# Optimization experiments

Measured on AMD Instinct MI355X. Metric: run time of the kernel, lower is better.

The kernel has to match this reference:

```python
import jax, jax.numpy as jnp
import numpy as np

B, TE, TD, D, U = 8, 256, 256, 256, 256


def setup_inputs() -> dict:
    key = jax.random.key(0)
    k1, k2, k3, k4, k5 = jax.random.split(key, 5)
    glorot = lambda k, shape: jax.random.uniform(
        k, shape, jnp.float32,
        -np.sqrt(6.0 / (shape[0] + shape[1])), np.sqrt(6.0 / (shape[0] + shape[1])))
    return {
        "en_seq": jax.random.normal(k1, (B, TE, D), jnp.float32),
        "de_seq": jax.random.normal(k2, (B, TD, D), jnp.float32),
        "w_en": glorot(k3, (D, U)),
        "w_de": glorot(k4, (D, U)),
        "nu": glorot(k5, (U, 1)),
    }


def reference(en_seq, de_seq, w_en, w_de, nu):
    # Additive co-attention scores.
    ae = jnp.einsum('bte,eu->btu', en_seq, w_en)          # (B, Te, U)
    ad = jnp.einsum('bsd,du->bsu', de_seq, w_de)          # (B, Td, U)
    # co_m[b, td, te, u] = ae[b, te, u] + ad[b, td, u]  (matches K.repeat / repeat_elements layout)
    co = jnp.tanh(ad[:, :, None, :] + ae[:, None, :, :])  # (B, Td, Te, U)
    mu = jnp.einsum('bstu,ul->bst', co, nu)               # (B, Td, Te)
    alphas = jax.nn.softmax(mu, axis=-1)                  # softmax over en time
    max_mu = jnp.max(mu, axis=-1)                         # (B, Td)
    max_alphas = jax.nn.softmax(max_mu, axis=-1)          # softmax over de time
    h_hat = jnp.sum(de_seq * max_alphas[..., None], axis=1)  # (B, Dd)
    sum_en = jnp.einsum('bst,bte->bse', alphas, en_seq)      # (B, Td, De)
    output = jnp.concatenate(
        [de_seq, sum_en, de_seq * sum_en, de_seq * h_hat[:, None, :]], axis=-1)
    return output  # (B, Td, 4*D)
```

## Files before the change

### kernel.cpp

```cpp
#include <hip/hip_runtime.h>

#define B_   8
#define TE_  256
#define TD_  256
#define D_   256
#define U_   256

#define AE_OFF    0
#define AD_OFF    524288
#define SUMEN_OFF 1048576
#define MAXMU_OFF 1572864

__device__ __forceinline__ float fexp2(float x) {
#if __has_builtin(__builtin_amdgcn_exp2f)
  return __builtin_amdgcn_exp2f(x);
#else
  return exp2f(x);
#endif
}
__device__ __forceinline__ float frcp(float x) {
#if __has_builtin(__builtin_amdgcn_rcpf)
  return __builtin_amdgcn_rcpf(x);
#else
  return 1.0f / x;
#endif
}

#define LOG2E_F 1.4426950408889634f
#define TWO_LOG2E_F 2.8853900817779268f

__global__ __launch_bounds__(256) void coatt_ka_proj(
    const float* __restrict__ en, const float* __restrict__ de,
    const float* __restrict__ w_en, const float* __restrict__ w_de,
    float* __restrict__ ws) {
  const int which = blockIdx.z;
  const float* __restrict__ A = which ? de : en;
  const float* __restrict__ W = which ? w_de : w_en;
  float* __restrict__ out = ws + (which ? AD_OFF : AE_OFF);
  const int rowBase = blockIdx.y * 64;
  const int colBase = blockIdx.x * 64;
  __shared__ float As[16][68];
  __shared__ float Bs[16][68];
  const int tid = threadIdx.x;
  const int tx = tid & 15, ty = tid >> 4;
  float acc[4][4] = {};
  for (int k0 = 0; k0 < D_; k0 += 16) {
    {
      const int r = tid >> 2;
      const int c = (tid & 3) * 4;
      const float4 a4 = *(const float4*)&A[(rowBase + r) * D_ + k0 + c];
      As[c + 0][r] = a4.x; As[c + 1][r] = a4.y;
      As[c + 2][r] = a4.z; As[c + 3][r] = a4.w;
      const int kk = tid >> 4;
      const int cc = (tid & 15) * 4;
      *(float4*)&Bs[kk][cc] = *(const float4*)&W[(k0 + kk) * U_ + colBase + cc];
    }
    __syncthreads();
#pragma unroll
    for (int k = 0; k < 16; ++k) {
      float av[4], bv[4];
      *(float4*)av = *(const float4*)&As[k][ty * 4];
      *(float4*)bv = *(const float4*)&Bs[k][tx * 4];
#pragma unroll
      for (int i = 0; i < 4; ++i)
#pragma unroll
        for (int j = 0; j < 4; ++j)
          acc[i][j] = fmaf(av[i], bv[j], acc[i][j]);
    }
    __syncthreads();
  }
#pragma unroll
  for (int i = 0; i < 4; ++i) {
    float4 o;
    o.x = fexp2(acc[i][0] * TWO_LOG2E_F);
    o.y = fexp2(acc[i][1] * TWO_LOG2E_F);
    o.z = fexp2(acc[i][2] * TWO_LOG2E_F);
    o.w = fexp2(acc[i][3] * TWO_LOG2E_F);
    *(float4*)&out[(rowBase + ty * 4 + i) * U_ + colBase + tx * 4] = o;
  }
}

__global__ __launch_bounds__(256) void coatt_kb_fused(
    const float* __restrict__ nu, const float* __restrict__ en,
    float* __restrict__ ws) {
  const float* __restrict__ Ee = ws + AE_OFF;
  const float* __restrict__ Ed = ws + AD_OFF;
  float* __restrict__ sum_en = ws + SUMEN_OFF;
  float* __restrict__ maxmu = ws + MAXMU_OFF;
  const int b = blockIdx.y;
  const int sBase = blockIdx.x * 4;
  const int tid = threadIdx.x;
  const int w = tid >> 6, lane = tid & 63;

  __shared__ float EdS[4][256];
  __shared__ float NUs[256];
  __shared__ float EeT[16][260];
  __shared__ float Mu[4][260];

  {
    const int r = tid >> 6, c4 = tid & 63;
    *(float4*)&EdS[r][c4 * 4] =
        *(const float4*)&Ed[(b * TD_ + sBase + r) * U_ + c4 * 4];
    NUs[tid] = -2.0f * nu[tid];
  }
  __syncthreads();

  float acc0 = 0.f, acc1 = 0.f, acc2 = 0.f, acc3 = 0.f;
  const int t = tid;
  for (int u0 = 0; u0 < U_; u0 += 16) {
#pragma unroll
    for (int k = 0; k < 4; ++k) {
      const int f = tid + 256 * k;
      const int tt = f >> 2, c = f & 3;
      const float4 v = *(const float4*)&Ee[(b * TE_ + tt) * U_ + u0 + c * 4];
      EeT[c * 4 + 0][tt] = v.x;
      EeT[c * 4 + 1][tt] = v.y;
      EeT[c * 4 + 2][tt] = v.z;
      EeT[c * 4 + 3][tt] = v.w;
    }
    __syncthreads();
#pragma unroll
    for (int uq = 0; uq < 4; ++uq) {
      float nv[4];
      *(float4*)nv = *(const float4*)&NUs[u0 + uq * 4];
      float ee[4];
#pragma unroll
      for (int j = 0; j < 4; ++j) ee[j] = EeT[uq * 4 + j][t];
      float e0[4], e1[4], e2[4], e3[4];
      *(float4*)e0 = *(const float4*)&EdS[0][u0 + uq * 4];
      *(float4*)e1 = *(const float4*)&EdS[1][u0 + uq * 4];
      *(float4*)e2 = *(const float4*)&EdS[2][u0 + uq * 4];
      *(float4*)e3 = *(const float4*)&EdS[3][u0 + uq * 4];
#pragma unroll
      for (int j = 0; j < 4; ++j) {
        acc0 = fmaf(nv[j], frcp(fmaf(e0[j], ee[j], 1.0f)), acc0);
        acc1 = fmaf(nv[j], frcp(fmaf(e1[j], ee[j], 1.0f)), acc1);
        acc2 = fmaf(nv[j], frcp(fmaf(e2[j], ee[j], 1.0f)), acc2);
        acc3 = fmaf(nv[j], frcp(fmaf(e3[j], ee[j], 1.0f)), acc3);
      }
    }
    __syncthreads();
  }

  Mu[0][t] = acc0;
  Mu[1][t] = acc1;
  Mu[2][t] = acc2;
  Mu[3][t] = acc3;
  __syncthreads();
  {
    float4 v = *(const float4*)&Mu[w][lane * 4];
    float m = fmaxf(fmaxf(v.x, v.y), fmaxf(v.z, v.w));
#pragma unroll
    for (int off = 32; off > 0; off >>= 1) m = fmaxf(m, __shfl_xor(m, off));
    float4 e;
    e.x = fexp2((v.x - m) * LOG2E_F);
    e.y = fexp2((v.y - m) * LOG2E_F);
    e.z = fexp2((v.z - m) * LOG2E_F);
    e.w = fexp2((v.w - m) * LOG2E_F);
    float sm = (e.x + e.y) + (e.z + e.w);
#pragma unroll
    for (int off = 32; off > 0; off >>= 1) sm += __shfl_xor(sm, off);
    const float inv = frcp(sm);
    e.x *= inv; e.y *= inv; e.z *= inv; e.w *= inv;
    *(float4*)&Mu[w][lane * 4] = e;
    if (lane == 0) maxmu[b * TD_ + sBase + w] = m;
  }
  __syncthreads();

  float4 p0 = {0, 0, 0, 0}, p1 = {0, 0, 0, 0}, p2 = {0, 0, 0, 0}, p3 = {0, 0, 0, 0};
  for (int t0 = 0; t0 < TE_; t0 += 16) {
#pragma unroll
    for (int k = 0; k < 4; ++k) {
      const int f = tid + 256 * k;
      const int r = f >> 6, c4 = f & 63;
      *(float4*)&EeT[r][c4 * 4] =
          *(const float4*)&en[(b * TE_ + t0 + r) * D_ + c4 * 4];
    }
    __syncthreads();
    float a0[4], a1[4], a2[4], a3[4];
    *(float4*)a0 = *(const float4*)&Mu[0][t0 + w * 4];
    *(float4*)a1 = *(const float4*)&Mu[1][t0 + w * 4];
    *(float4*)a2 = *(const float4*)&Mu[2][t0 + w * 4];
    *(float4*)a3 = *(const float4*)&Mu[3][t0 + w * 4];
#pragma unroll
    for (int j = 0; j < 4; ++j) {
      const float4 env = *(const float4*)&EeT[w * 4 + j][lane * 4];
      p0.x = fmaf(a0[j], env.x, p0.x); p0.y = fmaf(a0[j], env.y, p0.y);
      p0.z = fmaf(a0[j], env.z, p0.z); p0.w = fmaf(a0[j], env.w, p0.w);
      p1.x = fmaf(a1[j], env.x, p1.x); p1.y = fmaf(a1[j], env.y, p1.y);
      p1.z = fmaf(a1[j], env.z, p1.z); p1.w = fmaf(a1[j], env.w, p1.w);
      p2.x = fmaf(a2[j], env.x, p2.x); p2.y = fmaf(a2[j], env.y, p2.y);
      p2.z = fmaf(a2[j], env.z, p2.z); p2.w = fmaf(a2[j], env.w, p2.w);
      p3.x = fmaf(a3[j], env.x, p3.x); p3.y = fmaf(a3[j], env.y, p3.y);
      p3.z = fmaf(a3[j], env.z, p3.z); p3.w = fmaf(a3[j], env.w, p3.w);
    }
    __syncthreads();
  }
  {
    float* RED = &EeT[0][0];
    *(float4*)&RED[((w * 4 + 0) * 64 + lane) * 4] = p0;
    *(float4*)&RED[((w * 4 + 1) * 64 + lane) * 4] = p1;
    *(float4*)&RED[((w * 4 + 2) * 64 + lane) * 4] = p2;
    *(float4*)&RED[((w * 4 + 3) * 64 + lane) * 4] = p3;
    __syncthreads();
    const int s = tid >> 6, l = tid & 63;
    float4 sum = {0, 0, 0, 0};
#pragma unroll
    for (int ww = 0; ww < 4; ++ww) {
      const float4 q = *(const float4*)&RED[((ww * 4 + s) * 64 + l) * 4];
      sum.x += q.x; sum.y += q.y; sum.z += q.z; sum.w += q.w;
    }
    *(float4*)&sum_en[(b * TD_ + sBase + s) * D_ + l * 4] = sum;
  }
}

__global__ __launch_bounds__(256) void coatt_kc_out(
    const float* __restrict__ de, const float* __restrict__ ws,
    float* __restrict__ out) {
  const float* __restrict__ sum_en = ws + SUMEN_OFF;
  const float* __restrict__ maxmu = ws + MAXMU_OFF;
  const int b = blockIdx.y;
  const int sBase = blockIdx.x * 8;
  const int tid = threadIdx.x;
  const int w = tid >> 6, lane = tid & 63;
  __shared__ float malpha[256];
  __shared__ float red[8];
  __shared__ float hhL[256];
  const float v = maxmu[b * TD_ + tid];
  float m = v;
#pragma unroll
  for (int off = 32; off > 0; off >>= 1) m = fmaxf(m, __shfl_xor(m, off));
  if (lane == 0) red[w] = m;
  __syncthreads();
  m = fmaxf(fmaxf(red[0], red[1]), fmaxf(red[2], red[3]));
  const float e = fexp2((v - m) * LOG2E_F);
  float sm = e;
#pragma unroll
  for (int off = 32; off > 0; off >>= 1) sm += __shfl_xor(sm, off);
  if (lane == 0) red[4 + w] = sm;
  __syncthreads();
  sm = (red[4] + red[5]) + (red[6] + red[7]);
  malpha[tid] = e * frcp(sm);
  __syncthreads();
  float hh = 0.f;
#pragma unroll 8
  for (int s = 0; s < TD_; ++s)
    hh = fmaf(de[(b * TD_ + s) * D_ + tid], malpha[s], hh);
  hhL[tid] = hh;
  __syncthreads();
#pragma unroll
  for (int pass = 0; pass < 2; ++pass) {
    const int s = sBase + pass * 4 + w;
    const float4 d4 = *(const float4*)&de[(b * TD_ + s) * D_ + lane * 4];
    const float4 se4 = *(const float4*)&sum_en[(b * TD_ + s) * D_ + lane * 4];
    const float4 hh4 = *(const float4*)&hhL[lane * 4];
    float* o = out + (size_t)(b * TD_ + s) * (4 * D_);
    *(float4*)&o[lane * 4] = d4;
    *(float4*)&o[D_ + lane * 4] = se4;
    float4 pr;
    pr.x = d4.x * se4.x; pr.y = d4.y * se4.y;
    pr.z = d4.z * se4.z; pr.w = d4.w * se4.w;
    *(float4*)&o[2 * D_ + lane * 4] = pr;
    float4 q;
    q.x = d4.x * hh4.x; q.y = d4.y * hh4.y;
    q.z = d4.z * hh4.z; q.w = d4.w * hh4.w;
    *(float4*)&o[3 * D_ + lane * 4] = q;
  }
}

extern "C" void kernel_launch(void* const* d_in, const int* in_sizes, int n_in,
                              void* d_out, int out_size, void* d_ws, size_t ws_size,
                              hipStream_t stream) {
  (void)in_sizes; (void)n_in; (void)out_size; (void)ws_size;
  const float* en   = (const float*)d_in[0];
  const float* de   = (const float*)d_in[1];
  const float* w_en = (const float*)d_in[2];
  const float* w_de = (const float*)d_in[3];
  const float* nu   = (const float*)d_in[4];
  float* out = (float*)d_out;
  float* ws  = (float*)d_ws;

  coatt_ka_proj<<<dim3(4, 32, 2), 256, 0, stream>>>(en, de, w_en, w_de, ws);
  coatt_kb_fused<<<dim3(64, 8), 256, 0, stream>>>(nu, en, ws);
  coatt_kc_out<<<dim3(32, 8), 256, 0, stream>>>(de, ws, out);
}
```

Measured before the change: 132.4 us.

## Split fused attention kernel into mu/softmax, h-hat and output kernels with transposed Ee

The projection kernel now double-buffers 32-wide K tiles through registers and writes the encoder exponentials transposed (b,u,t), so the mu kernel reads them coalesced straight from global memory without LDS staging. The fused kernel is split into a mu+softmax kernel that writes alphas to workspace, an h-hat kernel parallelised over d, and an output kernel that computes sum_en from alphas and en, then writes all four output segments. This removes the LDS transposes and barriers and spreads the h-hat reduction over more blocks. In exchange it adds a kernel launch and a global round trip for alphas, and en is reread per block.

```diff
diff --git a/kernel.cpp b/kernel.cpp
--- a/kernel.cpp
+++ b/kernel.cpp
@@ -6,10 +6,11 @@
 #define D_   256
 #define U_   256
 
-#define AE_OFF    0
-#define AD_OFF    524288
-#define SUMEN_OFF 1048576
+#define EET_OFF   0
+#define ED_OFF    524288
+#define ALPHA_OFF 1048576
 #define MAXMU_OFF 1572864
+#define HH_OFF    1574912
 
 __device__ __forceinline__ float fexp2(float x) {
 #if __has_builtin(__builtin_amdgcn_exp2f)
@@ -29,203 +30,189 @@
 #define LOG2E_F 1.4426950408889634f
 #define TWO_LOG2E_F 2.8853900817779268f
 
-__global__ __launch_bounds__(256) void coatt_ka_proj(
+__global__ __launch_bounds__(256) void coatt_k1_proj(
     const float* __restrict__ en, const float* __restrict__ de,
     const float* __restrict__ w_en, const float* __restrict__ w_de,
     float* __restrict__ ws) {
   const int which = blockIdx.z;
   const float* __restrict__ A = which ? de : en;
   const float* __restrict__ W = which ? w_de : w_en;
-  float* __restrict__ out = ws + (which ? AD_OFF : AE_OFF);
   const int rowBase = blockIdx.y * 64;
   const int colBase = blockIdx.x * 64;
-  __shared__ float As[16][68];
-  __shared__ float Bs[16][68];
+  __shared__ float As[2][32][68];
+  __shared__ float Bs[2][32][68];
   const int tid = threadIdx.x;
   const int tx = tid & 15, ty = tid >> 4;
+
+  const int aRow0 = tid >> 3, aC4 = tid & 7;
+  const int bK0 = tid >> 4, bC4 = tid & 15;
+  float4 aR[2], bR[2];
+
+#pragma unroll
+  for (int kk = 0; kk < 2; ++kk) {
+    aR[kk] = *(const float4*)&A[(rowBase + aRow0 + 32 * kk) * D_ + aC4 * 4];
+    bR[kk] = *(const float4*)&W[(bK0 + 16 * kk) * U_ + colBase + bC4 * 4];
+  }
+#pragma unroll
+  for (int kk = 0; kk < 2; ++kk) {
+    float v[4]; *(float4*)v = aR[kk];
+#pragma unroll
+    for (int j = 0; j < 4; ++j) As[0][aC4 * 4 + j][aRow0 + 32 * kk] = v[j];
+    *(float4*)&Bs[0][bK0 + 16 * kk][bC4 * 4] = bR[kk];
+  }
+  __syncthreads();
+
   float acc[4][4] = {};
-  for (int k0 = 0; k0 < D_; k0 += 16) {
-    {
-      const int r = tid >> 2;
-      const int c = (tid & 3) * 4;
-      const float4 a4 = *(const float4*)&A[(rowBase + r) * D_ + k0 + c];
-      As[c + 0][r] = a4.x; As[c + 1][r] = a4.y;
-      As[c + 2][r] = a4.z; As[c + 3][r] = a4.w;
-      const int kk = tid >> 4;
-      const int cc = (tid & 15) * 4;
-      *(float4*)&Bs[kk][cc] = *(const float4*)&W[(k0 + kk) * U_ + colBase + cc];
+#define K1_COMPUTE(BUF)                                            \
+  _Pragma("unroll")                                                \
+  for (int k = 0; k < 32; ++k) {                                   \
+    float av[4], bv[4];                                            \
+    *(float4*)av = *(const float4*)&As[BUF][k][ty * 4];            \
+    *(float4*)bv = *(const float4*)&Bs[BUF][k][tx * 4];            \
+    _Pragma("unroll")                                              \
+    for (int i = 0; i < 4; ++i)                                    \
+      _Pragma("unroll")                                            \
+      for (int j = 0; j < 4; ++j)                                  \
+        acc[i][j] = fmaf(av[i], bv[j], acc[i][j]);                 \
+  }
+
+  for (int kc = 0; kc < 7; ++kc) {
+    const int k0 = (kc + 1) * 32;
+#pragma unroll
+    for (int kk = 0; kk < 2; ++kk) {
+      aR[kk] = *(const float4*)&A[(rowBase + aRow0 + 32 * kk) * D_ + k0 + aC4 * 4];
+      bR[kk] = *(const float4*)&W[(k0 + bK0 + 16 * kk) * U_ + colBase + bC4 * 4];
+    }
+    const int cur = kc & 1, nxt = cur ^ 1;
+    K1_COMPUTE(cur)
+#pragma unroll
+    for (int kk = 0; kk < 2; ++kk) {
+      float v[4]; *(float4*)v = aR[kk];
+#pragma unroll
+      for (int j = 0; j < 4; ++j) As[nxt][aC4 * 4 + j][aRow0 + 32 * kk] = v[j];
+      *(float4*)&Bs[nxt][bK0 + 16 * kk][bC4 * 4] = bR[kk];
     }
     __syncthreads();
-#pragma unroll
-    for (int k = 0; k < 16; ++k) {
-      float av[4], bv[4];
-      *(float4*)av = *(const float4*)&As[k][ty * 4];
-      *(float4*)bv = *(const float4*)&Bs[k][tx * 4];
-#pragma unroll
-      for (int i = 0; i < 4; ++i)
-#pragma unroll
-        for (int j = 0; j < 4; ++j)
-          acc[i][j] = fmaf(av[i], bv[j], acc[i][j]);
-    }
+  }
+  K1_COMPUTE(1)
+  __syncthreads();
+
+  if (which) {
+    float* __restrict__ out = ws + ED_OFF;
+#pragma unroll
+    for (int i = 0; i < 4; ++i) {
+      float4 o;
+      o.x = fexp2(acc[i][0] * TWO_LOG2E_F);
+      o.y = fexp2(acc[i][1] * TWO_LOG2E_F);
+      o.z = fexp2(acc[i][2] * TWO_LOG2E_F);
+      o.w = fexp2(acc[i][3] * TWO_LOG2E_F);
+      *(float4*)&out[(rowBase + ty * 4 + i) * U_ + colBase + tx * 4] = o;
+    }
+  } else {
+    float* Cs = &As[0][0][0];
+#pragma unroll
+    for (int i = 0; i < 4; ++i)
+#pragma unroll
+      for (int j = 0; j < 4; ++j)
+        Cs[(tx * 4 + j) * 68 + ty * 4 + i] = fexp2(acc[i][j] * TWO_LOG2E_F);
     __syncthreads();
-  }
-#pragma unroll
-  for (int i = 0; i < 4; ++i) {
-    float4 o;
-    o.x = fexp2(acc[i][0] * TWO_LOG2E_F);
-    o.y = fexp2(acc[i][1] * TWO_LOG2E_F);
-    o.z = fexp2(acc[i][2] * TWO_LOG2E_F);
-    o.w = fexp2(acc[i][3] * TWO_LOG2E_F);
-    *(float4*)&out[(rowBase + ty * 4 + i) * U_ + colBase + tx * 4] = o;
-  }
-}
-
-__global__ __launch_bounds__(256) void coatt_kb_fused(
-    const float* __restrict__ nu, const float* __restrict__ en,
-    float* __restrict__ ws) {
-  const float* __restrict__ Ee = ws + AE_OFF;
-  const float* __restrict__ Ed = ws + AD_OFF;
-  float* __restrict__ sum_en = ws + SUMEN_OFF;
+    float* __restrict__ out = ws + EET_OFF;
+    const int b = rowBase >> 8, t0 = rowBase & 255;
+#pragma unroll
+    for (int kk = 0; kk < 4; ++kk) {
+      const int q = tid + 256 * kk;
+      const int uc = q >> 4, tq = q & 15;
+      const float4 v = *(const float4*)&Cs[uc * 68 + tq * 4];
+      *(float4*)&out[(size_t)(b * U_ + colBase + uc) * TE_ + t0 + tq * 4] = v;
+    }
+  }
+}
+
+__global__ __launch_bounds__(256) void coatt_k2_mu(
+    const float* __restrict__ nu, float* __restrict__ ws) {
+  const float* __restrict__ EeT = ws + EET_OFF;
+  const float* __restrict__ Ed = ws + ED_OFF;
+  float* __restrict__ alphas = ws + ALPHA_OFF;
   float* __restrict__ maxmu = ws + MAXMU_OFF;
   const int b = blockIdx.y;
   const int sBase = blockIdx.x * 4;
   const int tid = threadIdx.x;
   const int w = tid >> 6, lane = tid & 63;
-
-  __shared__ float EdS[4][256];
-  __shared__ float NUs[256];
-  __shared__ float EeT[16][260];
-  __shared__ float Mu[4][260];
-
-  {
-    const int r = tid >> 6, c4 = tid & 63;
-    *(float4*)&EdS[r][c4 * 4] =
-        *(const float4*)&Ed[(b * TD_ + sBase + r) * U_ + c4 * 4];
-    NUs[tid] = -2.0f * nu[tid];
-  }
-  __syncthreads();
+  const float* __restrict__ Ee_b = EeT + (size_t)b * U_ * TE_ + tid;
+  const float* __restrict__ Ed_b = Ed + (size_t)(b * TD_ + sBase) * U_;
 
   float acc0 = 0.f, acc1 = 0.f, acc2 = 0.f, acc3 = 0.f;
-  const int t = tid;
-  for (int u0 = 0; u0 < U_; u0 += 16) {
-#pragma unroll
-    for (int k = 0; k < 4; ++k) {
-      const int f = tid + 256 * k;
-      const int tt = f >> 2, c = f & 3;
-      const float4 v = *(const float4*)&Ee[(b * TE_ + tt) * U_ + u0 + c * 4];
-      EeT[c * 4 + 0][tt] = v.x;
-      EeT[c * 4 + 1][tt] = v.y;
-      EeT[c * 4 + 2][tt] = v.z;
-      EeT[c * 4 + 3][tt] = v.w;
-    }
-    __syncthreads();
-#pragma unroll
-    for (int uq = 0; uq < 4; ++uq) {
-      float nv[4];
-      *(float4*)nv = *(const float4*)&NUs[u0 + uq * 4];
-      float ee[4];
-#pragma unroll
-      for (int j = 0; j < 4; ++j) ee[j] = EeT[uq * 4 + j][t];
-      float e0[4], e1[4], e2[4], e3[4];
-      *(float4*)e0 = *(const float4*)&EdS[0][u0 + uq * 4];
-      *(float4*)e1 = *(const float4*)&EdS[1][u0 + uq * 4];
-      *(float4*)e2 = *(const float4*)&EdS[2][u0 + uq * 4];
-      *(float4*)e3 = *(const float4*)&EdS[3][u0 + uq * 4];
-#pragma unroll
-      for (int j = 0; j < 4; ++j) {
-        acc0 = fmaf(nv[j], frcp(fmaf(e0[j], ee[j], 1.0f)), acc0);
-        acc1 = fmaf(nv[j], frcp(fmaf(e1[j], ee[j], 1.0f)), acc1);
-        acc2 = fmaf(nv[j], frcp(fmaf(e2[j], ee[j], 1.0f)), acc2);
-        acc3 = fmaf(nv[j], frcp(fmaf(e3[j], ee[j], 1.0f)), acc3);
-      }
-    }
-    __syncthreads();
-  }
-
-  Mu[0][t] = acc0;
-  Mu[1][t] = acc1;
-  Mu[2][t] = acc2;
-  Mu[3][t] = acc3;
-  __syncthreads();
-  {
-    float4 v = *(const float4*)&Mu[w][lane * 4];
-    float m = fmaxf(fmaxf(v.x, v.y), fmaxf(v.z, v.w));
-#pragma unroll
-    for (int off = 32; off > 0; off >>= 1) m = fmaxf(m, __shfl_xor(m, off));
-    float4 e;
-    e.x = fexp2((v.x - m) * LOG2E_F);
-    e.y = fexp2((v.y - m) * LOG2E_F);
-    e.z = fexp2((v.z - m) * LOG2E_F);
-    e.w = fexp2((v.w - m) * LOG2E_F);
-    float sm = (e.x + e.y) + (e.z + e.w);
-#pragma unroll
-    for (int off = 32; off > 0; off >>= 1) sm += __shfl_xor(sm, off);
-    const float inv = frcp(sm);
-    e.x *= inv; e.y *= inv; e.z *= inv; e.w *= inv;
-    *(float4*)&Mu[w][lane * 4] = e;
-    if (lane == 0) maxmu[b * TD_ + sBase + w] = m;
-  }
-  __syncthreads();
-
-  float4 p0 = {0, 0, 0, 0}, p1 = {0, 0, 0, 0}, p2 = {0, 0, 0, 0}, p3 = {0, 0, 0, 0};
-  for (int t0 = 0; t0 < TE_; t0 += 16) {
-#pragma unroll
-    for (int k = 0; k < 4; ++k) {
-      const int f = tid + 256 * k;
-      const int r = f >> 6, c4 = f & 63;
-      *(float4*)&EeT[r][c4 * 4] =
-          *(const float4*)&en[(b * TE_ + t0 + r) * D_ + c4 * 4];
-    }
-    __syncthreads();
-    float a0[4], a1[4], a2[4], a3[4];
-    *(float4*)a0 = *(const float4*)&Mu[0][t0 + w * 4];
-    *(float4*)a1 = *(const float4*)&Mu[1][t0 + w * 4];
-    *(float4*)a2 = *(const float4*)&Mu[2][t0 + w * 4];
-    *(float4*)a3 = *(const float4*)&Mu[3][t0 + w * 4];
+#pragma unroll 4
+  for (int u4 = 0; u4 < 64; ++u4) {
+    const float4 nv = *(const float4*)&nu[u4 * 4];
+    const float4 e0 = *(const float4*)&Ed_b[0 * U_ + u4 * 4];
+    const float4 e1 = *(const float4*)&Ed_b[1 * U_ + u4 * 4];
+    const float4 e2 = *(const float4*)&Ed_b[2 * U_ + u4 * 4];
+    const float4 e3 = *(const float4*)&Ed_b[3 * U_ + u4 * 4];
+    float ee[4];
+#pragma unroll
+    for (int j = 0; j < 4; ++j) ee[j] = Ee_b[(u4 * 4 + j) * TE_];
+    const float* nvp = (const float*)&nv;
+    const float* p0 = (const float*)&e0;
+    const float* p1 = (const float*)&e1;
+    const float* p2 = (const float*)&e2;
+    const float* p3 = (const float*)&e3;
 #pragma unroll
     for (int j = 0; j < 4; ++j) {
-      const float4 env = *(const float4*)&EeT[w * 4 + j][lane * 4];
-      p0.x = fmaf(a0[j], env.x, p0.x); p0.y = fmaf(a0[j], env.y, p0.y);
-      p0.z = fmaf(a0[j], env.z, p0.z); p0.w = fmaf(a0[j], env.w, p0.w);
-      p1.x = fmaf(a1[j], env.x, p1.x); p1.y = fmaf(a1[j], env.y, p1.y);
-      p1.z = fmaf(a1[j], env.z, p1.z); p1.w = fmaf(a1[j], env.w, p1.w);
-      p2.x = fmaf(a2[j], env.x, p2.x); p2.y = fmaf(a2[j], env.y, p2.y);
-      p2.z = fmaf(a2[j], env.z, p2.z); p2.w = fmaf(a2[j], env.w, p2.w);
-      p3.x = fmaf(a3[j], env.x, p3.x); p3.y = fmaf(a3[j], env.y, p3.y);
-      p3.z = fmaf(a3[j], env.z, p3.z); p3.w = fmaf(a3[j], env.w, p3.w);
-    }
-    __syncthreads();
-  }
-  {
-    float* RED = &EeT[0][0];
-    *(float4*)&RED[((w * 4 + 0) * 64 + lane) * 4] = p0;
-    *(float4*)&RED[((w * 4 + 1) * 64 + lane) * 4] = p1;
-    *(float4*)&RED[((w * 4 + 2) * 64 + lane) * 4] = p2;
-    *(float4*)&RED[((w * 4 + 3) * 64 + lane) * 4] = p3;
-    __syncthreads();
-    const int s = tid >> 6, l = tid & 63;
-    float4 sum = {0, 0, 0, 0};
-#pragma unroll
-    for (int ww = 0; ww < 4; ++ww) {
-      const float4 q = *(const float4*)&RED[((ww * 4 + s) * 64 + l) * 4];
-      sum.x += q.x; sum.y += q.y; sum.z += q.z; sum.w += q.w;
-    }
-    *(float4*)&sum_en[(b * TD_ + sBase + s) * D_ + l * 4] = sum;
-  }
-}
-
-__global__ __launch_bounds__(256) void coatt_kc_out(
-    const float* __restrict__ de, const float* __restrict__ ws,
-    float* __restrict__ out) {
-  const float* __restrict__ sum_en = ws + SUMEN_OFF;
+      acc0 = fmaf(nvp[j], frcp(fmaf(p0[j], ee[j], 1.0f)), acc0);
+      acc1 = fmaf(nvp[j], frcp(fmaf(p1[j], ee[j], 1.0f)), acc1);
+      acc2 = fmaf(nvp[j], frcp(fmaf(p2[j], ee[j], 1.0f)), acc2);
+      acc3 = fmaf(nvp[j], frcp(fmaf(p3[j], ee[j], 1.0f)), acc3);
+    }
+  }
+  float v[4] = {-2.f * acc0, -2.f * acc1, -2.f * acc2, -2.f * acc3};
+  __shared__ float part[4][4];
+  float m[4];
+#pragma unroll
+  for (int s = 0; s < 4; ++s) {
+    m[s] = v[s];
+#pragma unroll
+    for (int off = 32; off > 0; off >>= 1) m[s] = fmaxf(m[s], __shfl_xor(m[s], off));
+    if (lane == 0) part[s][w] = m[s];
+  }
+  __syncthreads();
+#pragma unroll
+  for (int s = 0; s < 4; ++s)
+    m[s] = fmaxf(fmaxf(part[s][0], part[s][1]), fmaxf(part[s][2], part[s][3]));
+  __syncthreads();
+  float e[4], sm[4];
+#pragma unroll
+  for (int s = 0; s < 4; ++s) {
+    e[s] = fexp2((v[s] - m[s]) * LOG2E_F);
+    sm[s] = e[s];
+#pragma unroll
+    for (int off = 32; off > 0; off >>= 1) sm[s] += __shfl_xor(sm[s], off);
+    if (lane == 0) part[s][w] = sm[s];
+  }
+  __syncthreads();
+  float* __restrict__ al = alphas + (size_t)(b * TD_ + sBase) * TE_;
+#pragma unroll
+  for (int s = 0; s < 4; ++s) {
+    const float tot = (part[s][0] + part[s][1]) + (part[s][2] + part[s][3]);
+    al[s * TE_ + tid] = e[s] * frcp(tot);
+  }
+  if (tid == 0) {
+#pragma unroll
+    for (int s = 0; s < 4; ++s) maxmu[b * TD_ + sBase + s] = m[s];
+  }
+}
+
+__global__ __launch_bounds__(256) void coatt_k3_hhat(
+    const float* __restrict__ de, float* __restrict__ ws) {
   const float* __restrict__ maxmu = ws + MAXMU_OFF;
+  float* __restrict__ hhat = ws + HH_OFF;
   const int b = blockIdx.y;
-  const int sBase = blockIdx.x * 8;
+  const int dBase = blockIdx.x * 32;
   const int tid = threadIdx.x;
   const int w = tid >> 6, lane = tid & 63;
+  __shared__ float red[8];
   __shared__ float malpha[256];
-  __shared__ float red[8];
-  __shared__ float hhL[256];
+  __shared__ float acc_red[256];
   const float v = maxmu[b * TD_ + tid];
   float m = v;
 #pragma unroll
@@ -242,29 +229,63 @@
   sm = (red[4] + red[5]) + (red[6] + red[7]);
   malpha[tid] = e * frcp(sm);
   __syncthreads();
-  float hh = 0.f;
-#pragma unroll 8
-  for (int s = 0; s < TD_; ++s)
-    hh = fmaf(de[(b * TD_ + s) * D_ + tid], malpha[s], hh);
-  hhL[tid] = hh;
-  __syncthreads();
-#pragma unroll
-  for (int pass = 0; pass < 2; ++pass) {
-    const int s = sBase + pass * 4 + w;
-    const float4 d4 = *(const float4*)&de[(b * TD_ + s) * D_ + lane * 4];
-    const float4 se4 = *(const float4*)&sum_en[(b * TD_ + s) * D_ + lane * 4];
-    const float4 hh4 = *(const float4*)&hhL[lane * 4];
-    float* o = out + (size_t)(b * TD_ + s) * (4 * D_);
-    *(float4*)&o[lane * 4] = d4;
-    *(float4*)&o[D_ + lane * 4] = se4;
-    float4 pr;
-    pr.x = d4.x * se4.x; pr.y = d4.y * se4.y;
-    pr.z = d4.z * se4.z; pr.w = d4.w * se4.w;
-    *(float4*)&o[2 * D_ + lane * 4] = pr;
-    float4 q;
-    q.x = d4.x * hh4.x; q.y = d4.y * hh4.y;
-    q.z = d4.z * hh4.z; q.w = d4.w * hh4.w;
-    *(float4*)&o[3 * D_ + lane * 4] = q;
+  const int dl = tid & 31, sg = tid >> 5;
+  float acc = 0.f;
+  for (int s = sg * 32; s < sg * 32 + 32; ++s)
+    acc = fmaf(de[(b * TD_ + s) * D_ + dBase + dl], malpha[s], acc);
+  acc_red[tid] = acc;
+  __syncthreads();
+  if (tid < 32) {
+    float t = acc_red[tid];
+#pragma unroll
+    for (int g = 1; g < 8; ++g) t += acc_red[g * 32 + tid];
+    hhat[b * D_ + dBase + tid] = t;
+  }
+}
+
+__global__ __launch_bounds__(256) void coatt_k4_out(
+    const float* __restrict__ en, const float* __restrict__ de,
+    const float* __restrict__ ws, float* __restrict__ out) {
+  const float* __restrict__ alphas = ws + ALPHA_OFF;
+  const float* __restrict__ hhat = ws + HH_OFF;
+  const int b = blockIdx.y;
+  const int sBase = blockIdx.x * 4;
+  const int d = threadIdx.x;
+  const float* __restrict__ al = alphas + (size_t)(b * TD_ + sBase) * TE_;
+  const float* __restrict__ en_b = en + (size_t)b * TE_ * D_ + d;
+
+  float acc0 = 0.f, acc1 = 0.f, acc2 = 0.f, acc3 = 0.f;
+#pragma unroll 4
+  for (int t4 = 0; t4 < 64; ++t4) {
+    const float4 a0 = *(const float4*)&al[0 * TE_ + t4 * 4];
+    const float4 a1 = *(const float4*)&al[1 * TE_ + t4 * 4];
+    const float4 a2 = *(const float4*)&al[2 * TE_ + t4 * 4];
+    const float4 a3 = *(const float4*)&al[3 * TE_ + t4 * 4];
+    float env[4];
+#pragma unroll
+    for (int j = 0; j < 4; ++j) env[j] = en_b[(t4 * 4 + j) * D_];
+    const float* q0 = (const float*)&a0;
+    const float* q1 = (const float*)&a1;
+    const float* q2 = (const float*)&a2;
+    const float* q3 = (const float*)&a3;
+#pragma unroll
+    for (int j = 0; j < 4; ++j) {
+      acc0 = fmaf(q0[j], env[j], acc0);
+      acc1 = fmaf(q1[j], env[j], acc1);
+      acc2 = fmaf(q2[j], env[j], acc2);
+      acc3 = fmaf(q3[j], env[j], acc3);
+    }
+  }
+  const float hh = hhat[b * D_ + d];
+  const float se[4] = {acc0, acc1, acc2, acc3};
+#pragma unroll
+  for (int s = 0; s < 4; ++s) {
+    const float dd = de[(size_t)(b * TD_ + sBase + s) * D_ + d];
+    float* o = out + (size_t)(b * TD_ + sBase + s) * (4 * D_);
+    o[d] = dd;
+    o[D_ + d] = se[s];
+    o[2 * D_ + d] = dd * se[s];
+    o[3 * D_ + d] = dd * hh;
   }
 }
 
@@ -280,7 +301,8 @@
   float* out = (float*)d_out;
   float* ws  = (float*)d_ws;
 
-  coatt_ka_proj<<<dim3(4, 32, 2), 256, 0, stream>>>(en, de, w_en, w_de, ws);
-  coatt_kb_fused<<<dim3(64, 8), 256, 0, stream>>>(nu, en, ws);
-  coatt_kc_out<<<dim3(32, 8), 256, 0, stream>>>(de, ws, out);
-}
+  coatt_k1_proj<<<dim3(4, 32, 2), 256, 0, stream>>>(en, de, w_en, w_de, ws);
+  coatt_k2_mu<<<dim3(64, 8), 256, 0, stream>>>(nu, ws);
+  coatt_k3_hhat<<<dim3(8, 8), 256, 0, stream>>>(de, ws);
+  coatt_k4_out<<<dim3(64, 8), 256, 0, stream>>>(en, de, ws, out);
+}
```

Measured after the change: 121.9 us. -7.9%, faster.
